# Performance work log

Measured on AMD Instinct MI355X. Metric: run time of the kernel, lower is better.

The kernel has to match this reference:

```python
import jax, jax.numpy as jnp
import numpy as np

HEAD_NUM = 16

def setup_inputs() -> dict:
    key = jax.random.key(0)
    ks = jax.random.split(key, 5)
    B, N, D = 2, 2048, 1024
    x = jax.random.normal(ks[0], (B, N, D), dtype=jnp.float32)
    scale = 0.02
    W_q = jax.random.normal(ks[1], (D, D), dtype=jnp.float32) * scale
    W_k = jax.random.normal(ks[2], (D, D), dtype=jnp.float32) * scale
    W_v = jax.random.normal(ks[3], (D, D), dtype=jnp.float32) * scale
    W_o = jax.random.normal(ks[4], (D, D), dtype=jnp.float32) * scale
    return {"x": x, "W_q": W_q, "W_k": W_k, "W_v": W_v, "W_o": W_o}

def reference(x, W_q, W_k, W_v, W_o):
    B, N, D = x.shape
    H = HEAD_NUM
    hd = D // H  # head_dim
    inv_sqrt_hd = 1.0 / np.sqrt(hd).astype(np.float32)

    def split_head(t):
        # einops 'b n (d h) -> b h n d' : head index is the INNER factor
        return t.reshape(B, N, hd, H).transpose(0, 3, 1, 2)  # [B,H,N,hd]

    # nn.Linear(bias=False): y = x @ W.T
    Q = split_head(x @ W_q.T)
    K = split_head(x @ W_k.T)
    V = split_head(x @ W_v.T)

    scores = jnp.einsum('bhnd,bhmd->bhnm', Q, K) * inv_sqrt_hd  # [B,H,N,N]
    attn = jax.nn.softmax(scores, axis=-1)
    heads = jnp.einsum('bhnm,bhmd->bhnd', attn, V)  # [B,H,N,hd]

    # einops 'b h n d -> b n (h d)' : head index is the OUTER factor here
    concat = heads.transpose(0, 2, 1, 3).reshape(B, N, D)
    return concat @ W_o.T
```

## Files before the change

### kernel.cpp

```cpp
#include <hip/hip_runtime.h>
#include <hip/hip_bf16.h>

typedef __bf16 bf16_t;
typedef __attribute__((ext_vector_type(8))) __bf16 bf16x8;
typedef __attribute__((ext_vector_type(4))) __bf16 bf16x4;
typedef __attribute__((ext_vector_type(4))) float f32x4;
typedef __attribute__((ext_vector_type(16))) float f32x16;

#define MFMA16(A,B,C) __builtin_amdgcn_mfma_f32_16x16x32_bf16((A),(B),(C),0,0,0)
#define MFMA32(A,B,C) __builtin_amdgcn_mfma_f32_32x32x16_bf16((A),(B),(C),0,0,0)

#define BATCH 2
#define SEQ 2048
#define DMODEL 1024
#define NHEAD 16
#define HDIM 64
#define MROWS (BATCH * SEQ)

__device__ __forceinline__ void async16(const bf16_t* g, bf16_t* l) {
    __builtin_amdgcn_global_load_lds(
        (const __attribute__((address_space(1))) unsigned int*)g,
        (__attribute__((address_space(3))) unsigned int*)l, 16, 0, 0);
}

__device__ __forceinline__ bf16x8 ldsA32(const bf16_t* base, int row, int chunk) {
    return *(const bf16x8*)&base[row * 32 + ((chunk ^ ((row >> 1) & 3)) << 3)];
}

__device__ __forceinline__ unsigned pk(float a, float b) {
    union { unsigned u; bf16_t h[2]; } t;
    t.h[0] = (bf16_t)a;
    t.h[1] = (bf16_t)b;
    return t.u;
}

__device__ __forceinline__ void plane32_swap(unsigned& d, unsigned& s) {
    asm("v_permlane32_swap_b32 %0, %1" : "+v"(d), "+v"(s));
}

__device__ __forceinline__ void sm_pack(const f32x16& st, float* rsp, bf16x8* pf) {
    float pexp[16];
#pragma unroll
    for (int r = 0; r < 16; ++r)
        pexp[r] = __builtin_amdgcn_exp2f(st[r]);
    rsp[0] += pexp[0] + pexp[4] + pexp[8] + pexp[12];
    rsp[1] += pexp[1] + pexp[5] + pexp[9] + pexp[13];
    rsp[2] += pexp[2] + pexp[6] + pexp[10] + pexp[14];
    rsp[3] += pexp[3] + pexp[7] + pexp[11] + pexp[15];
#pragma unroll
    for (int s1 = 0; s1 < 2; ++s1) {
        unsigned lo01 = pk(pexp[8 * s1 + 0], pexp[8 * s1 + 1]);
        unsigned lo23 = pk(pexp[8 * s1 + 2], pexp[8 * s1 + 3]);
        unsigned hi01 = pk(pexp[8 * s1 + 4], pexp[8 * s1 + 5]);
        unsigned hi23 = pk(pexp[8 * s1 + 6], pexp[8 * s1 + 7]);
        plane32_swap(lo01, hi01);
        plane32_swap(lo23, hi23);
        union { bf16x8 v; unsigned u[4]; } outv;
        outv.u[0] = lo01;
        outv.u[1] = lo23;
        outv.u[2] = hi01;
        outv.u[3] = hi23;
        pf[s1] = outv.v;
    }
}

__global__ void split_kernel(const float* __restrict__ x, const float* __restrict__ Wq,
                             const float* __restrict__ Wk, const float* __restrict__ Wv,
                             const float* __restrict__ Wo, bf16_t* __restrict__ xh,
                             bf16_t* __restrict__ wh) {
    int blk = blockIdx.x;
    if (blk < 4096) {
        int i = blk * 256 + threadIdx.x;
        f32x4 v = ((const f32x4*)x)[i];
        bf16x4 h;
#pragma unroll
        for (int c = 0; c < 4; ++c) h[c] = (bf16_t)v[c];
        ((bf16x4*)xh)[i] = h;
        return;
    }
    int e = blk - 4096;
    int z = e >> 10;
    int i = (e & 1023) * 256 + threadIdx.x;
    const float* src = (z == 0) ? Wq : (z == 1) ? Wk : (z == 2) ? Wv : Wo;
    const float scale = (z == 0) ? 0.125f * 1.44269504088896f : 1.0f;
    int row = i >> 8, col4 = i & 255;
    int r_src;
    if (z < 3) {
        int h = row >> 6, d = row & 63;
        r_src = 16 * d + h;
    } else {
        r_src = row;
    }
    f32x4 v = ((const f32x4*)src)[r_src * 256 + col4];
    bf16x4 h4;
#pragma unroll
    for (int c = 0; c < 4; ++c) h4[c] = (bf16_t)(v[c] * scale);
    ((bf16x4*)(wh + (size_t)z * DMODEL * DMODEL))[i] = h4;
}

__global__ __launch_bounds__(256)
void gemm_qkv_kernel(const bf16_t* __restrict__ Ah, const bf16_t* __restrict__ Bh0,
                     bf16_t* __restrict__ Coh0, bf16_t* __restrict__ Vt,
                     int M, int Nn, int Kk) {
    __shared__ __align__(16) bf16_t smem[2][8192];

    const int id = blockIdx.x;
    const int xcd = id & 7;
    const int t = id >> 3;
    const int n0i = t & 7;
    const int u = t >> 3;
    const int z = u >> 2;
    const int m0g = u & 3;
    const int m0 = (m0g * 8 + xcd) * 128;
    const int n0 = n0i * 128;

    const bf16_t* Bh = Bh0 + (size_t)z * Nn * Kk;
    const int tid = threadIdx.x;
    const int wave = tid >> 6, lane = tid & 63, lq = lane >> 4, ln = lane & 15;
    const int wr = wave >> 1, wc = wave & 1;

    const bf16_t* g_ptr[4];
    int l_off[4];
#pragma unroll
    for (int q = 0; q < 4; ++q) {
        int e = wave * 4 + q;
        int a = e >> 3, uu = e & 7;
        int C = uu * 64 + lane;
        int r = C >> 2, p = C & 3;
        int c = p ^ ((r >> 1) & 3);
        g_ptr[q] = (a == 0 ? Ah + (size_t)(m0 + r) * Kk
                           : Bh + (size_t)(n0 + r) * Kk) + c * 8;
        l_off[q] = a * 4096 + uu * 512;
    }

    f32x4 acc[4][4] = {};

#pragma unroll
    for (int q = 0; q < 4; ++q)
        async16(g_ptr[q], &smem[0][l_off[q]]);

    const int NIT = Kk / 32;
    for (int j = 0; j < NIT; ++j) {
        __syncthreads();
        if (j + 1 < NIT) {
#pragma unroll
            for (int q = 0; q < 4; ++q)
                async16(g_ptr[q] + (j + 1) * 32, &smem[(j + 1) & 1][l_off[q]]);
        }
        const bf16_t* cur = smem[j & 1];

        bf16x8 ah[4], bh[4];
#pragma unroll
        for (int tt = 0; tt < 4; ++tt) {
            ah[tt] = ldsA32(cur, wr * 64 + tt * 16 + ln, lq);
            bh[tt] = ldsA32(cur + 4096, wc * 64 + tt * 16 + ln, lq);
        }
#pragma unroll
        for (int tm = 0; tm < 4; ++tm)
#pragma unroll
            for (int tn = 0; tn < 4; ++tn)
                acc[tm][tn] = MFMA16(ah[tm], bh[tn], acc[tm][tn]);
    }

    if (z != 2) {
#pragma unroll
        for (int tm = 0; tm < 4; ++tm)
#pragma unroll
            for (int tn = 0; tn < 4; ++tn)
#pragma unroll
                for (int p = 0; p < 4; ++p) {
                    int gm = m0 + wr * 64 + tm * 16 + lq * 4 + p;
                    int gn = n0 + wc * 64 + tn * 16 + ln;
                    Coh0[(size_t)z * M * Nn + (size_t)gm * Nn + gn] =
                        (bf16_t)acc[tm][tn][p];
                }
    } else {
#pragma unroll
        for (int tm = 0; tm < 4; ++tm)
#pragma unroll
            for (int tn = 0; tn < 4; ++tn) {
                int gn = n0 + wc * 64 + tn * 16 + ln;
                int hh = gn >> 6, dd = gn & 63;
                int gm0 = m0 + wr * 64 + tm * 16 + lq * 4;
                int bb = gm0 >> 11, nn = gm0 & 2047;
                bf16x4 v4;
#pragma unroll
                for (int p = 0; p < 4; ++p) v4[p] = (bf16_t)acc[tm][tn][p];
                *(bf16x4*)&Vt[(((size_t)(bb * NHEAD + hh)) * HDIM + dd) * SEQ + nn] = v4;
            }
    }
}

__global__ __launch_bounds__(256)
void gemm_out_kernel(const bf16_t* __restrict__ Ah, const bf16_t* __restrict__ Bh,
                     float* __restrict__ Cf, int M, int Nn, int Kk) {
    __shared__ __align__(16) bf16_t smem[2][6144];

    const int id = blockIdx.x;
    const int xcd = id & 7;
    const int t = id >> 3;
    const int n0i = t & 7;
    const int m0g = t >> 3;
    const int m0 = (m0g * 8 + xcd) * 64;
    const int n0 = n0i * 128;

    const int tid = threadIdx.x;
    const int wave = tid >> 6, lane = tid & 63, lq = lane >> 4, ln = lane & 15;
    const int wr = wave >> 1, wc = wave & 1;

    const bf16_t* g_ptr[3];
    int l_off[3];
#pragma unroll
    for (int q = 0; q < 3; ++q) {
        int e = wave * 3 + q;
        const bf16_t* arr;
        int u, rowbase, lb;
        if (e < 4) { arr = Ah; u = e;     rowbase = m0; lb = 0; }
        else       { arr = Bh; u = e - 4; rowbase = n0; lb = 2048; }
        int r = u * 16 + (lane >> 2), p = lane & 3;
        int c = p ^ ((r >> 1) & 3);
        g_ptr[q] = arr + (size_t)(rowbase + r) * Kk + c * 8;
        l_off[q] = lb + u * 512;
    }

    f32x4 acc[2][4] = {};

#pragma unroll
    for (int q = 0; q < 3; ++q)
        async16(g_ptr[q], &smem[0][l_off[q]]);

    const int NIT = Kk / 32;
    for (int j = 0; j < NIT; ++j) {
        __syncthreads();
        if (j + 1 < NIT) {
#pragma unroll
            for (int q = 0; q < 3; ++q)
                async16(g_ptr[q] + (j + 1) * 32, &smem[(j + 1) & 1][l_off[q]]);
        }
        const bf16_t* cur = smem[j & 1];

        bf16x8 ah[2], bh[4];
#pragma unroll
        for (int tt = 0; tt < 2; ++tt)
            ah[tt] = ldsA32(cur, wr * 32 + tt * 16 + ln, lq);
#pragma unroll
        for (int tt = 0; tt < 4; ++tt)
            bh[tt] = ldsA32(cur + 2048, wc * 64 + tt * 16 + ln, lq);
#pragma unroll
        for (int tm = 0; tm < 2; ++tm)
#pragma unroll
            for (int tn = 0; tn < 4; ++tn)
                acc[tm][tn] = MFMA16(ah[tm], bh[tn], acc[tm][tn]);
    }

#pragma unroll
    for (int tm = 0; tm < 2; ++tm)
#pragma unroll
        for (int tn = 0; tn < 4; ++tn)
#pragma unroll
            for (int p = 0; p < 4; ++p) {
                int gm = m0 + wr * 32 + tm * 16 + lq * 4 + p;
                int gn = n0 + wc * 64 + tn * 16 + ln;
                Cf[(size_t)gm * Nn + gn] = acc[tm][tn][p];
            }
}

__global__ __launch_bounds__(512, 1)
void attn_kernel(const bf16_t* __restrict__ Qh, const bf16_t* __restrict__ Kh,
                 const bf16_t* __restrict__ Vt, bf16_t* __restrict__ Ch) {
    __shared__ __align__(16) bf16_t smem[2][2][8192];

    const int id = blockIdx.x;
    const int bh = ((id >> 6) << 3) | (id & 7);
    const int qt = (id >> 3) & 7;
    const int b = bh >> 4, h = bh & 15;
    const int q0 = qt * 256;
    const int tid = threadIdx.x;
    const int g = tid >> 8;
    const int wv = (tid >> 6) & 3;
    const int lane = tid & 63;
    const int ln32 = lane & 31, hl = lane >> 5;

    bf16x8 qfh[2][4];
#pragma unroll
    for (int qs = 0; qs < 2; ++qs) {
        size_t qrow = ((size_t)(b * SEQ + q0 + wv * 64 + qs * 32 + ln32)) * DMODEL +
                      h * HDIM + hl * 8;
#pragma unroll
        for (int c = 0; c < 4; ++c)
            qfh[qs][c] = *(const bf16x8*)&Qh[qrow + c * 16];
    }

    const int xrow = ln32 * 64;
    int xc[4];
#pragma unroll
    for (int c = 0; c < 4; ++c)
        xc[c] = (((2 * c + hl) ^ (ln32 & 7)) << 3) + xrow;

    bf16_t* gsm = &smem[g][0][0];
    const bf16_t* g_cur[4];
    int l_off[4];
    size_t g_step[4];
#pragma unroll
    for (int q = 0; q < 4; ++q) {
        int e = wv * 4 + q;
        int a = e >> 3, u = e & 7;
        int r = u * 8 + (lane >> 3), p = lane & 7;
        int c = p ^ (r & 7);
        if (a == 0) {
            g_cur[q] = Kh + ((size_t)(b * SEQ + g * 1024 + r)) * DMODEL +
                       h * HDIM + c * 8;
            l_off[q] = u * 512;
            g_step[q] = (size_t)64 * DMODEL;
        } else {
            g_cur[q] = Vt + ((size_t)(bh * HDIM + r)) * SEQ + g * 1024 + c * 8;
            l_off[q] = 4096 + u * 512;
            g_step[q] = 64;
        }
    }

    f32x16 o[2][2];
#pragma unroll
    for (int qs = 0; qs < 2; ++qs)
#pragma unroll
        for (int dt = 0; dt < 2; ++dt)
#pragma unroll
            for (int r = 0; r < 16; ++r) o[qs][dt][r] = 0.0f;
    float rsA[4] = {0.f, 0.f, 0.f, 0.f};
    float rsB[4] = {0.f, 0.f, 0.f, 0.f};

#pragma unroll
    for (int q = 0; q < 4; ++q) {
        async16(g_cur[q], gsm + l_off[q]);
        g_cur[q] += g_step[q];
    }

    for (int j = 0; j < 16; ++j) {
        __syncthreads();
        if (j < 15) {
#pragma unroll
            for (int q = 0; q < 4; ++q) {
                async16(g_cur[q], gsm + ((j + 1) & 1) * 8192 + l_off[q]);
                g_cur[q] += g_step[q];
            }
        }
        const bf16_t* Kc = gsm + (j & 1) * 8192;
        const bf16_t* Vc = Kc + 4096;

        bf16x8 pfA[4], pfB[4];
#pragma unroll
        for (int kt = 0; kt < 2; ++kt) {
            bf16x8 kh[4];
#pragma unroll
            for (int c = 0; c < 4; ++c)
                kh[c] = *(const bf16x8*)&Kc[kt * 2048 + xc[c]];
            f32x16 s0, s1;
#pragma unroll
            for (int r = 0; r < 16; ++r) { s0[r] = 0.0f; s1[r] = 0.0f; }
            __builtin_amdgcn_s_setprio(1);
#pragma unroll
            for (int c = 0; c < 4; ++c)
                s0 = MFMA32(kh[c], qfh[0][c], s0);
#pragma unroll
            for (int c = 0; c < 4; ++c)
                s1 = MFMA32(kh[c], qfh[1][c], s1);
            __builtin_amdgcn_s_setprio(0);
            sm_pack(s0, rsA, &pfA[kt * 2]);
            sm_pack(s1, rsB, &pfB[kt * 2]);
        }
        __builtin_amdgcn_s_setprio(1);
#pragma unroll
        for (int s = 0; s < 4; ++s) {
            bf16x8 va0 = *(const bf16x8*)&Vc[xc[s]];
            bf16x8 va1 = *(const bf16x8*)&Vc[2048 + xc[s]];
            o[0][0] = MFMA32(va0, pfA[s], o[0][0]);
            o[0][1] = MFMA32(va1, pfA[s], o[0][1]);
            o[1][0] = MFMA32(va0, pfB[s], o[1][0]);
            o[1][1] = MFMA32(va1, pfB[s], o[1][1]);
        }
        __builtin_amdgcn_s_setprio(0);
    }

    float rs[2];
    rs[0] = (rsA[0] + rsA[1]) + (rsA[2] + rsA[3]);
    rs[1] = (rsB[0] + rsB[1]) + (rsB[2] + rsB[3]);
#pragma unroll
    for (int qs = 0; qs < 2; ++qs)
        rs[qs] += __shfl_xor(rs[qs], 32);

    __syncthreads();
    float* cbuf = (float*)smem;
    float* rbuf = cbuf + 8192;
#pragma unroll
    for (int dt = 0; dt < 2; ++dt) {
        if (g == 1) {
#pragma unroll
            for (int qs = 0; qs < 2; ++qs)
#pragma unroll
                for (int r = 0; r < 16; ++r) {
                    int d = (r & 3) + 8 * (r >> 2) + 4 * hl;
                    cbuf[d * 256 + wv * 64 + qs * 32 + ln32] = o[qs][dt][r];
                }
            if (dt == 0 && hl == 0) {
                rbuf[wv * 64 + ln32] = rs[0];
                rbuf[wv * 64 + 32 + ln32] = rs[1];
            }
        }
        __syncthreads();
        if (g == 0) {
#pragma unroll
            for (int qs = 0; qs < 2; ++qs) {
#pragma unroll
                for (int r = 0; r < 16; ++r) {
                    int d = (r & 3) + 8 * (r >> 2) + 4 * hl;
                    o[qs][dt][r] += cbuf[d * 256 + wv * 64 + qs * 32 + ln32];
                }
                if (dt == 0) rs[qs] += rbuf[wv * 64 + qs * 32 + ln32];
            }
        }
        __syncthreads();
    }
    float inv[2];
    inv[0] = (g == 0) ? 1.0f / rs[0] : 0.0f;
    inv[1] = (g == 0) ? 1.0f / rs[1] : 0.0f;

    float* fbuf = (float*)smem;
#pragma unroll
    for (int dh = 0; dh < 2; ++dh) {
        if (g == 0) {
#pragma unroll
            for (int qs = 0; qs < 2; ++qs)
#pragma unroll
                for (int r = 0; r < 16; ++r) {
                    int d_loc = (r & 3) + 8 * (r >> 2) + 4 * hl;
                    fbuf[(wv * 64 + qs * 32 + ln32) * 33 + d_loc] =
                        o[qs][dh][r] * inv[qs];
                }
        }
        __syncthreads();
        {
            int gw = tid >> 6;
#pragma unroll
            for (int qq = 0; qq < 16; ++qq) {
                int qrow = gw * 32 + hl * 16 + qq;
                float v = fbuf[qrow * 33 + ln32];
                size_t gidx = ((size_t)(b * SEQ + q0 + qrow)) * DMODEL +
                              h * HDIM + dh * 32 + ln32;
                Ch[gidx] = (bf16_t)v;
            }
        }
        __syncthreads();
    }
}

extern "C" void kernel_launch(void* const* d_in, const int* in_sizes, int n_in,
                              void* d_out, int out_size, void* d_ws, size_t ws_size,
                              hipStream_t stream) {
    const float* x  = (const float*)d_in[0];
    const float* Wq = (const float*)d_in[1];
    const float* Wk = (const float*)d_in[2];
    const float* Wv = (const float*)d_in[3];
    const float* Wo = (const float*)d_in[4];
    float* out = (float*)d_out;

    char* ws = (char*)d_ws;
    size_t off = 0;
    auto alloc = [&](size_t bytes) -> bf16_t* {
        bf16_t* p = (bf16_t*)(ws + off);
        off += (bytes + 255) & ~(size_t)255;
        return p;
    };
    const size_t XE = (size_t)MROWS * DMODEL;
    const size_t WE = (size_t)DMODEL * DMODEL;

    bf16_t* xh  = alloc(XE * 2);
    bf16_t* wh  = alloc(4 * WE * 2);
    bf16_t* qnh = alloc(3 * XE * 2);
    bf16_t* vth = alloc(XE * 2);
    bf16_t* ch  = alloc(XE * 2);
    (void)ws_size; (void)in_sizes; (void)n_in; (void)out_size;

    split_kernel<<<8192, 256, 0, stream>>>(x, Wq, Wk, Wv, Wo, xh, wh);

    gemm_qkv_kernel<<<768, 256, 0, stream>>>(xh, wh, qnh, vth, MROWS, DMODEL, DMODEL);

    attn_kernel<<<256, 512, 0, stream>>>(qnh, qnh + XE, vth, ch);

    gemm_out_kernel<<<512, 256, 0, stream>>>(ch, wh + 3 * WE, out, MROWS, DMODEL, DMODEL);
}
```

Baseline: 172.3 us.

## Triple-buffer K/V tiles and software-pipeline QK softmax ahead of PV

The attention loop moves from double to triple buffering of K/V tiles in LDS. It computes QK^T plus softmax packing for tile j+1 before the PV MFMAs of tile j, so the two phases can overlap across iterations. Barriers become explicit vmcnt waits with s_barrier and sched_barrier, and the score accumulator starts by passing a zero register instead of zeroing it each time. This raises LDS use, extends register live ranges for the two sets of P fragments, and relies on the hand-written waitcnt logic being correct.

```diff
diff --git a/kernel.cpp b/kernel.cpp
--- a/kernel.cpp
+++ b/kernel.cpp
@@ -268,7 +268,7 @@
 __global__ __launch_bounds__(512, 1)
 void attn_kernel(const bf16_t* __restrict__ Qh, const bf16_t* __restrict__ Kh,
                  const bf16_t* __restrict__ Vt, bf16_t* __restrict__ Ch) {
-    __shared__ __align__(16) bf16_t smem[2][2][8192];
+    __shared__ __align__(16) bf16_t smem[2][3][8192];
 
     const int id = blockIdx.x;
     const int bh = ((id >> 6) << 3) | (id & 7);
@@ -326,60 +326,76 @@
         for (int dt = 0; dt < 2; ++dt)
 #pragma unroll
             for (int r = 0; r < 16; ++r) o[qs][dt][r] = 0.0f;
+    f32x16 zacc;
+#pragma unroll
+    for (int r = 0; r < 16; ++r) zacc[r] = 0.0f;
     float rsA[4] = {0.f, 0.f, 0.f, 0.f};
     float rsB[4] = {0.f, 0.f, 0.f, 0.f};
 
-#pragma unroll
-    for (int q = 0; q < 4; ++q) {
-        async16(g_cur[q], gsm + l_off[q]);
-        g_cur[q] += g_step[q];
-    }
-
-    for (int j = 0; j < 16; ++j) {
-        __syncthreads();
-        if (j < 15) {
-#pragma unroll
-            for (int q = 0; q < 4; ++q) {
-                async16(g_cur[q], gsm + ((j + 1) & 1) * 8192 + l_off[q]);
-                g_cur[q] += g_step[q];
-            }
-        }
-        const bf16_t* Kc = gsm + (j & 1) * 8192;
-        const bf16_t* Vc = Kc + 4096;
-
-        bf16x8 pfA[4], pfB[4];
+    auto QKPACK = [&](const bf16_t* Kc, bf16x8* pfAo, bf16x8* pfBo) {
 #pragma unroll
         for (int kt = 0; kt < 2; ++kt) {
             bf16x8 kh[4];
 #pragma unroll
             for (int c = 0; c < 4; ++c)
                 kh[c] = *(const bf16x8*)&Kc[kt * 2048 + xc[c]];
-            f32x16 s0, s1;
-#pragma unroll
-            for (int r = 0; r < 16; ++r) { s0[r] = 0.0f; s1[r] = 0.0f; }
             __builtin_amdgcn_s_setprio(1);
-#pragma unroll
-            for (int c = 0; c < 4; ++c)
-                s0 = MFMA32(kh[c], qfh[0][c], s0);
-#pragma unroll
-            for (int c = 0; c < 4; ++c)
-                s1 = MFMA32(kh[c], qfh[1][c], s1);
+            f32x16 s0 = MFMA32(kh[0], qfh[0][0], zacc);
+            f32x16 s1 = MFMA32(kh[0], qfh[1][0], zacc);
+#pragma unroll
+            for (int c = 1; c < 4; ++c) s0 = MFMA32(kh[c], qfh[0][c], s0);
+#pragma unroll
+            for (int c = 1; c < 4; ++c) s1 = MFMA32(kh[c], qfh[1][c], s1);
             __builtin_amdgcn_s_setprio(0);
-            sm_pack(s0, rsA, &pfA[kt * 2]);
-            sm_pack(s1, rsB, &pfB[kt * 2]);
-        }
+            sm_pack(s0, rsA, &pfAo[kt * 2]);
+            sm_pack(s1, rsB, &pfBo[kt * 2]);
+        }
+    };
+    auto PV = [&](const bf16_t* Vc, const bf16x8* pfAi, const bf16x8* pfBi) {
         __builtin_amdgcn_s_setprio(1);
 #pragma unroll
         for (int s = 0; s < 4; ++s) {
             bf16x8 va0 = *(const bf16x8*)&Vc[xc[s]];
             bf16x8 va1 = *(const bf16x8*)&Vc[2048 + xc[s]];
-            o[0][0] = MFMA32(va0, pfA[s], o[0][0]);
-            o[0][1] = MFMA32(va1, pfA[s], o[0][1]);
-            o[1][0] = MFMA32(va0, pfB[s], o[1][0]);
-            o[1][1] = MFMA32(va1, pfB[s], o[1][1]);
+            o[0][0] = MFMA32(va0, pfAi[s], o[0][0]);
+            o[0][1] = MFMA32(va1, pfAi[s], o[0][1]);
+            o[1][0] = MFMA32(va0, pfBi[s], o[1][0]);
+            o[1][1] = MFMA32(va1, pfBi[s], o[1][1]);
         }
         __builtin_amdgcn_s_setprio(0);
-    }
+    };
+    auto ISSUE = [&](int bufi) {
+#pragma unroll
+        for (int q = 0; q < 4; ++q)
+            async16(g_cur[q], gsm + bufi * 8192 + l_off[q]);
+    };
+    auto ADVANCE = [&]() {
+#pragma unroll
+        for (int q = 0; q < 4; ++q) g_cur[q] += g_step[q];
+    };
+
+    ISSUE(0); ADVANCE();
+    ISSUE(1); ADVANCE();
+    asm volatile("s_waitcnt vmcnt(4)" ::: "memory");
+    __builtin_amdgcn_s_barrier();
+    __builtin_amdgcn_sched_barrier(0);
+    bf16x8 pfAc[4], pfBc[4];
+    QKPACK(gsm + 0 * 8192, pfAc, pfBc);
+
+#pragma unroll 3
+    for (int j = 0; j < 15; ++j) {
+        asm volatile("s_waitcnt vmcnt(0)" ::: "memory");
+        __builtin_amdgcn_s_barrier();
+        __builtin_amdgcn_sched_barrier(0);
+        ISSUE((j + 2) % 3);
+        if (j + 2 < 15) ADVANCE();
+        bf16x8 pfAn[4], pfBn[4];
+        QKPACK(gsm + ((j + 1) % 3) * 8192, pfAn, pfBn);
+        PV(gsm + (j % 3) * 8192 + 4096, pfAc, pfBc);
+#pragma unroll
+        for (int i = 0; i < 4; ++i) { pfAc[i] = pfAn[i]; pfBc[i] = pfBn[i]; }
+    }
+    PV(gsm + 0 * 8192 + 4096, pfAc, pfBc);
 
     float rs[2];
     rs[0] = (rsA[0] + rsA[1]) + (rsA[2] + rsA[3]);
```

After: 246.5 us. 1.43x slower.
